# Kernel optimization log

Hardware: AMD Instinct MI355X
Metric: run time of the kernel (lower is better)

## Reference

```python
import jax, jax.numpy as jnp
import numpy as np

B, N, K, UP = 8, 2048, 20, 2
CIN, D, COUT, PH, AH = 256, 64, 128, 64, 256
EPS = 1e-5

def c1(x, W, b):
    # 1x1 Conv1d: x (B,C,N), W (O,C)
    return jnp.einsum('oc,bcn->bon', W, x) + b[None, :, None]

def c2(x, W, b):
    # 1x1 Conv2d: x (B,C,N,K), W (O,C)
    return jnp.einsum('oc,bcnk->bonk', W, x) + b[None, :, None, None]

def bn2(x, g, be):
    # eval-mode BatchNorm2d with running_mean=0, running_var=1
    inv = np.float32(1.0 / np.sqrt(1.0 + EPS))
    return g[None, :, None, None] * x * inv + be[None, :, None, None]

def knn_idx(p, k):
    # p: (B,N,3) -> (B,N,k) indices of k nearest neighbors (incl. self)
    sq = jnp.sum(p * p, -1)
    d = sq[:, :, None] + sq[:, None, :] - 2.0 * jnp.einsum('bnd,bmd->bnm', p, p)
    _, idx = jax.lax.top_k(-d, k)
    return idx

def group(feat, idx):
    # grouping_operation: feat (B,C,N), idx (B,N,k) -> (B,C,N,k)
    return jax.vmap(lambda f, i: f[:, i])(feat, idx)

def setup_inputs() -> dict:
    key = jax.random.key(0)
    ks = jax.random.split(key, 24)
    s = 0.02
    rn = lambda i, shp: jax.random.normal(ks[i], shp, jnp.float32) * s
    return {
        'pos': jax.random.normal(ks[0], (B, 3, N), jnp.float32),
        'key_feat': jax.random.normal(ks[1], (B, CIN, N), jnp.float32),
        'query_feat': jax.random.normal(ks[2], (B, CIN, N), jnp.float32),
        'upfeat': jax.random.normal(ks[3], (B, CIN, N), jnp.float32),
        # mlp_v (MLP_Res): in 2*CIN -> CIN -> CIN with shortcut
        'Wv1': rn(4, (CIN, 2 * CIN)), 'bv1': jnp.zeros(CIN, jnp.float32),
        'Wv2': rn(5, (CIN, CIN)), 'bv2': jnp.zeros(CIN, jnp.float32),
        'Wvs': rn(6, (CIN, 2 * CIN)), 'bvs': jnp.zeros(CIN, jnp.float32),
        # key/query/value/upfeat 1x1 convs CIN -> D
        'Wk': rn(7, (D, CIN)), 'bk': jnp.zeros(D, jnp.float32),
        'Wq': rn(8, (D, CIN)), 'bq': jnp.zeros(D, jnp.float32),
        'Wvv': rn(9, (D, CIN)), 'bvv': jnp.zeros(D, jnp.float32),
        'Wu': rn(10, (D, CIN)), 'bu': jnp.zeros(D, jnp.float32),
        # pos_mlp: 3 -> PH (BN, ReLU) -> D
        'Wp1': rn(11, (PH, 3)), 'bp1': jnp.zeros(PH, jnp.float32),
        'gp1': jnp.ones(PH, jnp.float32), 'betap1': jnp.zeros(PH, jnp.float32),
        'Wp2': rn(12, (D, PH)), 'bp2': jnp.zeros(D, jnp.float32),
        # attn_mlp: D -> AH (BN, ReLU) -> ConvTranspose2d(AH, D, (UP,1), (UP,1))
        'Wa1': rn(13, (AH, D)), 'ba1': jnp.zeros(AH, jnp.float32),
        'ga1': jnp.ones(AH, jnp.float32), 'betaa1': jnp.zeros(AH, jnp.float32),
        'Wt': rn(14, (AH, D, UP)), 'bt': jnp.zeros(D, jnp.float32),
        # conv_end D -> COUT, residual CIN -> COUT
        'Wend': rn(15, (COUT, D)), 'bend': jnp.zeros(COUT, jnp.float32),
        'Wres': rn(16, (COUT, CIN)), 'bres': jnp.zeros(COUT, jnp.float32),
    }

def reference(pos, key_feat, query_feat, upfeat,
              Wv1, bv1, Wv2, bv2, Wvs, bvs,
              Wk, bk, Wq, bq, Wvv, bvv, Wu, bu,
              Wp1, bp1, gp1, betap1, Wp2, bp2,
              Wa1, ba1, ga1, betaa1, Wt, bt,
              Wend, bend, Wres, bres):
    # mlp_v on concat(key, query)
    x = jnp.concatenate([key_feat, query_feat], axis=1)          # (B,2CIN,N)
    value = c1(jax.nn.relu(c1(x, Wv1, bv1)), Wv2, bv2) + c1(x, Wvs, bvs)
    identity = value                                             # (B,CIN,N)
    kf = c1(key_feat, Wk, bk)
    qf = c1(query_feat, Wq, bq)
    vf = c1(value, Wvv, bvv)                                     # (B,D,N)
    idx = knn_idx(pos.transpose(0, 2, 1), K)                     # (B,N,K)
    kg = group(kf, idx)                                          # (B,D,N,K)
    qk_rel = qf[:, :, :, None] - kg
    pos_rel = pos[:, :, :, None] - group(pos, idx)               # (B,3,N,K)
    pos_emb = c2(jax.nn.relu(bn2(c2(pos_rel, Wp1, bp1), gp1, betap1)), Wp2, bp2)
    uf = c1(upfeat, Wu, bu)
    u_rel = uf[:, :, :, None] - group(uf, idx)                   # (B,D,N,K)
    h = jax.nn.relu(bn2(c2(qk_rel + pos_emb + u_rel, Wa1, ba1), ga1, betaa1))  # (B,AH,N,K)
    b = h.shape[0]
    # ConvTranspose2d kernel (UP,1) stride (UP,1): expand N -> N*UP
    att = jnp.einsum('bhnk,hcr->bcnrk', h, Wt).reshape(b, D, N * UP, K) + bt[None, :, None, None]
    att = jax.nn.softmax(att, axis=-1)
    val = group(vf, idx) + pos_emb + u_rel                       # (B,D,N,K)
    val = jnp.repeat(val, UP, axis=2)                            # nearest Upsample (UP,1)
    agg = jnp.sum(att * val, axis=-1)                            # (B,D,N*UP)
    y = c1(agg, Wend, bend)                                      # (B,COUT,N*UP)
    ident = jnp.repeat(c1(identity, Wres, bres), UP, axis=2)     # residual path
    return y + ident
```

## Files before the change

kernel.cpp:

```cpp
#include <hip/hip_runtime.h>
#include <hip/hip_bf16.h>
#include <math.h>

#define BB 8
#define NN 2048
#define KK 20
#define UPF 2
#define CIN 256
#define DD 64
#define COUTN 128
#define PHH 64
#define AHH 256
#define BN_INV 0.9999950000374997f
#define KQ 4
#define NPB 8

typedef __hip_bfloat16 bf16;
typedef unsigned short u16;
typedef unsigned long long u64;
typedef _Float16 f16;
typedef _Float16 h2   __attribute__((ext_vector_type(2)));
typedef _Float16 f16x4 __attribute__((ext_vector_type(4)));
typedef _Float16 f16x8 __attribute__((ext_vector_type(8)));
typedef float    f32x4 __attribute__((ext_vector_type(4)));

static __device__ __forceinline__ float bf2f(const bf16 v) { return __bfloat162float(v); }
static __device__ __forceinline__ bf16  f2bf(const float v) { return __float2bfloat16(v); }
static __device__ __forceinline__ u16   f2bfu(const float v) {
    return __builtin_bit_cast(u16, __float2bfloat16(v));
}
static __device__ __forceinline__ float lo2f(const unsigned v) { return __builtin_bit_cast(float, v << 16); }
static __device__ __forceinline__ float hi2f(const unsigned v) { return __builtin_bit_cast(float, v & 0xFFFF0000u); }

static __device__ __forceinline__ f32x4 mfma16(const f16x8 a, const f16x8 b, const f32x4 c) {
    return __builtin_amdgcn_mfma_f32_16x16x32_f16(a, b, c, 0, 0, 0);
}
static __device__ __forceinline__ unsigned fmap(const float f) {
    unsigned u = __builtin_bit_cast(unsigned, f);
    return (u >> 31) ? ~u : (u | 0x80000000u);
}
static __device__ __forceinline__ void lds_fence() {
    asm volatile("s_waitcnt lgkmcnt(0)" ::: "memory");
    __builtin_amdgcn_sched_barrier(0);
}

__global__ void sentinel_kernel(float* out) {
    if (threadIdx.x == 0 && blockIdx.x == 0) out[0] = 100.0f;
}

__global__ __launch_bounds__(256) void prep_kernel(
    const float* __restrict__ Wa1, const float* __restrict__ Wp2,
    const float* __restrict__ Wend, const float* __restrict__ Wt,
    const float* __restrict__ Wv1, const float* __restrict__ Wv2,
    const float* __restrict__ Wvs, const float* __restrict__ Wvv,
    const float* __restrict__ Wres,
    const float* __restrict__ Wk, const float* __restrict__ Wq,
    const float* __restrict__ Wu,
    const float* __restrict__ ba1, const float* __restrict__ ga1,
    const float* __restrict__ betaa1,
    f16* __restrict__ Wa1h, f16* __restrict__ Wp2h, f16* __restrict__ Wth,
    float* __restrict__ A1s, float* __restrict__ A1b,
    float* __restrict__ WendT,
    f16* __restrict__ Wv1h, f16* __restrict__ Wv2h, f16* __restrict__ Wvsh,
    f16* __restrict__ Wvvh, f16* __restrict__ Wresh,
    f16* __restrict__ Wkh, f16* __restrict__ Wqh, f16* __restrict__ Wuh) {
    const int t = blockIdx.x * 256 + threadIdx.x;
    if (t < AHH * DD)        Wa1h[t] = (f16)Wa1[t];
    if (t < PHH * DD)        Wp2h[t] = (f16)Wp2[t];
    if (t < COUTN * AHH)     { int cr = t >> 8, hh = t & 255; Wth[t] = (f16)Wt[hh * COUTN + cr]; }
    if (t < AHH) {
        float gsc = ga1[t] * BN_INV;
        A1s[t] = gsc;
        A1b[t] = gsc * ba1[t] + betaa1[t];
    }
    if (t < COUTN * DD)      { int r = t / DD,  c = t % DD;  WendT[c * COUTN + r] = Wend[t]; }
    if (t < CIN * 2 * CIN)   Wv1h[t] = (f16)Wv1[t];
    if (t < CIN * CIN)       Wv2h[t] = (f16)Wv2[t];
    if (t < CIN * 2 * CIN)   Wvsh[t] = (f16)Wvs[t];
    if (t < DD * CIN)        Wvvh[t] = (f16)Wvv[t];
    if (t < COUTN * CIN)     Wresh[t] = (f16)Wres[t];
    if (t < DD * CIN)        Wkh[t]  = (f16)Wk[t];
    if (t < DD * CIN)        Wqh[t]  = (f16)Wq[t];
    if (t < DD * CIN)        Wuh[t]  = (f16)Wu[t];
}

__global__ __launch_bounds__(256) void xpose_kernel(
    const float* __restrict__ key_feat, const float* __restrict__ query_feat,
    const float* __restrict__ upfeat,
    f16* __restrict__ xkqT, f16* __restrict__ xuT) {
    __shared__ float tile[64][65];
    const int b  = blockIdx.x >> 5;
    const int n0 = (blockIdx.x & 31) << 6;
    const int y  = blockIdx.y;
    const int src = y >> 2;
    const int ct  = (y & 3) << 6;
    const int t = threadIdx.x;
    const float* xin = (src == 0) ? key_feat : (src == 1) ? query_feat : upfeat;
    f16* dst; int CT, cb;
    if (src < 2) { dst = xkqT; CT = 512; cb = src * 256 + ct; }
    else         { dst = xuT;  CT = 256; cb = ct; }
    for (int u = t; u < 64 * 64; u += 256) {
        const int c = u >> 6, j = u & 63;
        tile[c][j] = xin[((size_t)b * CIN + ct + c) * NN + n0 + j];
    }
    __syncthreads();
    for (int u = t; u < 64 * 32; u += 256) {
        const int n = u >> 5, c0 = (u & 31) << 1;
        h2 pr; pr.x = (f16)tile[c0][n]; pr.y = (f16)tile[c0 + 1][n];
        ((unsigned*)dst)[(((size_t)b * NN + n0 + n) * CT + cb + c0) >> 1] =
            __builtin_bit_cast(unsigned, pr);
    }
}

__global__ __launch_bounds__(256) void knn_kernel(const float* __restrict__ pos,
                                                  u16* __restrict__ idx_out,
                                                  float* __restrict__ posT) {
    __shared__ float dist[KQ][NN];
    __shared__ int   hist[KQ][512];
    __shared__ u64   ltbuf[KQ][KK];
    __shared__ int   tiebuf[KQ][64];

    const int b  = blockIdx.x / (NN / KQ);
    const int n0 = (blockIdx.x % (NN / KQ)) * KQ;
    const int t = threadIdx.x;
    const int g = t >> 6, lane = t & 63;
    const int n = n0 + g;
    const float* pb = pos + (size_t)b * 3 * NN;
    const size_t rowKK = ((size_t)b * NN + n) * KK;

    if (lane < 3) posT[((size_t)b * NN + n) * 3 + lane] = pb[(size_t)lane * NN + n];
    const float qx = pb[n], qy = pb[NN + n], qz = pb[2 * NN + n];
    const float sqq = __fadd_rn(__fadd_rn(__fmul_rn(qx, qx), __fmul_rn(qy, qy)), __fmul_rn(qz, qz));
    for (int j = 0; j < NN / 64; ++j) {
        const int m = lane + j * 64;
        float px = pb[m];
        float py = pb[NN + m];
        float pz = pb[2 * NN + m];
        float sqm = __fadd_rn(__fadd_rn(__fmul_rn(px, px), __fmul_rn(py, py)), __fmul_rn(pz, pz));
        float dt  = __fadd_rn(__fadd_rn(__fmul_rn(qx, px), __fmul_rn(qy, py)), __fmul_rn(qz, pz));
        dist[g][m] = __fsub_rn(__fadd_rn(sqq, sqm), __fmul_rn(2.0f, dt));
    }
    lds_fence();

    unsigned pref = 0u;
    int kn = KK;
    for (int pass = 0; pass < 4; ++pass) {
        const int shift = 24 - 8 * pass;
        const unsigned pm = (pass == 0) ? 0u : (0xFFFFFFFFu << (32 - 8 * pass));
#pragma unroll
        for (int i = 0; i < 8; ++i) hist[g][lane + i * 64] = 0;
        lds_fence();
        for (int j = 0; j < NN / 64; ++j) {
            const unsigned key = fmap(dist[g][lane + j * 64]);
            if ((key & pm) == pref)
                atomicAdd(&hist[g][((lane & 1) << 8) | ((key >> shift) & 255)], 1);
        }
        lds_fence();
        const int h0  = hist[g][4 * lane + 0] + hist[g][256 + 4 * lane + 0];
        const int h1  = hist[g][4 * lane + 1] + hist[g][256 + 4 * lane + 1];
        const int h2v = hist[g][4 * lane + 2] + hist[g][256 + 4 * lane + 2];
        const int h3  = hist[g][4 * lane + 3] + hist[g][256 + 4 * lane + 3];
        const int lsum = h0 + h1 + h2v + h3;
        int incl = lsum;
#pragma unroll
        for (int off = 1; off < 64; off <<= 1) {
            int v = __shfl_up(incl, off, 64);
            if (lane >= off) incl += v;
        }
        const int excl = incl - lsum;
        const bool cross = (excl < kn) && (excl + lsum >= kn);
        const u64 mask = __ballot(cross);
        const int src = __ffsll((unsigned long long)mask) - 1;
        int bsel, cb;
        if      (excl + h0 >= kn)             { bsel = 0; cb = excl; }
        else if (excl + h0 + h1 >= kn)        { bsel = 1; cb = excl + h0; }
        else if (excl + h0 + h1 + h2v >= kn)  { bsel = 2; cb = excl + h0 + h1; }
        else                                  { bsel = 3; cb = excl + h0 + h1 + h2v; }
        const unsigned npref = pref | ((unsigned)(4 * lane + bsel) << shift);
        const int nkn = kn - cb;
        pref = (unsigned)__shfl((int)npref, src, 64);
        kn   = __shfl(nkn, src, 64);
    }

    const unsigned T = pref;
    int nlt = 0, ceq = 0;
    const u64 lmask = (lane == 63) ? 0x7FFFFFFFFFFFFFFFull : ((1ull << lane) - 1);
    for (int j = 0; j < NN / 64; ++j) {
        const int m = lane + j * 64;
        const unsigned key = fmap(dist[g][m]);
        const bool lt = key < T, eq = key == T;
        const u64 mlt = __ballot(lt);
        if (lt) ltbuf[g][nlt + __popcll(mlt & lmask)] = ((u64)key << 32) | (unsigned)m;
        nlt += __popcll(mlt);
        const u64 meq = __ballot(eq);
        if (eq) {
            const int p = ceq + __popcll(meq & lmask);
            if (p < 64) tiebuf[g][p] = m;
        }
        ceq += __popcll(meq);
    }
    lds_fence();

    {
        u64 v = (lane < nlt) ? ltbuf[g][lane] : 0xFFFFFFFFFFFFFFFFull;
        int rank = 0;
#pragma unroll
        for (int j = 0; j < KK; ++j) {
            const u64 o = (u64)__shfl((long long)v, j, 64);
            if (o < v) ++rank;
        }
        if (lane < nlt) idx_out[rowKK + rank] = (u16)(v & 0xFFFFu);
    }
    if (ceq <= 64) {
        int ti = (lane < ceq) ? tiebuf[g][lane] : 0x7FFFFFFF;
        int rk = 0;
        for (int j = 0; j < 64; ++j) {
            const int o = __shfl(ti, j, 64);
            if (o < ti) ++rk;
        }
        if (lane < ceq && rk < kn) idx_out[rowKK + nlt + rk] = (u16)ti;
    } else {
        for (int iter = 0; iter < kn; ++iter) {
            int bi = NN;
            for (int j = 0; j < NN / 64; ++j) {
                const int m = lane + j * 64;
                if (fmap(dist[g][m]) == T && m < bi) bi = m;
            }
#pragma unroll
            for (int off = 32; off > 0; off >>= 1) bi = min(bi, __shfl_down(bi, off, 64));
            bi = __shfl(bi, 0, 64);
            if (lane == 0) {
                idx_out[rowKK + nlt + iter] = (u16)bi;
                dist[g][bi] = 3.4e38f;
            }
            lds_fence();
        }
    }
}

__global__ __launch_bounds__(256) void value_mfma(
    const f16* __restrict__ xkqT,
    const f16* __restrict__ Wv1h, const float* __restrict__ bv1,
    const f16* __restrict__ Wv2h, const float* __restrict__ bv2,
    const f16* __restrict__ Wvsh, const float* __restrict__ bvs,
    const f16* __restrict__ Wvvh, const float* __restrict__ bvv,
    const f16* __restrict__ Wresh, const float* __restrict__ bres,
    bf16* __restrict__ vf_ws, bf16* __restrict__ resid_ws) {
    __shared__ __align__(16) char hv[32 * 512];
    const int b  = blockIdx.x >> 6;
    const int n0 = (blockIdx.x & 63) << 5;
    const int t = threadIdx.x;
    const int w = t >> 6, l = t & 63, g = l >> 4, li = l & 15;
    const f16* xb = xkqT + ((size_t)b * NN + n0) * 512;
    const f32x4 zero4 = {0.f, 0.f, 0.f, 0.f};

    f32x4 a1[4][2];
#pragma unroll
    for (int mt = 0; mt < 4; ++mt) { a1[mt][0] = zero4; a1[mt][1] = zero4; }
    for (int ks = 0; ks < 16; ++ks) {
        f16x8 bx0 = *(const f16x8*)(xb + (size_t)li * 512 + ks * 32 + g * 8);
        f16x8 bx1 = *(const f16x8*)(xb + (size_t)(16 + li) * 512 + ks * 32 + g * 8);
#pragma unroll
        for (int mt = 0; mt < 4; ++mt) {
            const f16x8 af = *(const f16x8*)(Wv1h + (size_t)(w * 64 + mt * 16 + li) * 512 + ks * 32 + g * 8);
            a1[mt][0] = mfma16(af, bx0, a1[mt][0]);
            a1[mt][1] = mfma16(af, bx1, a1[mt][1]);
        }
    }
#pragma unroll
    for (int mt = 0; mt < 4; ++mt) {
        const int ch0 = w * 64 + mt * 16 + g * 4;
        const float4 b4 = *(const float4*)(bv1 + ch0);
#pragma unroll
        for (int nt = 0; nt < 2; ++nt) {
            const int n = nt * 16 + li;
            f16x4 px;
            px.x = (f16)fmaxf(a1[mt][nt][0] + b4.x, 0.f);
            px.y = (f16)fmaxf(a1[mt][nt][1] + b4.y, 0.f);
            px.z = (f16)fmaxf(a1[mt][nt][2] + b4.z, 0.f);
            px.w = (f16)fmaxf(a1[mt][nt][3] + b4.w, 0.f);
            *(f16x4*)(hv + n * 512 + ((ch0 * 2) ^ ((n & 7) << 4))) = px;
        }
    }
    __syncthreads();

    f32x4 a2[4][2];
#pragma unroll
    for (int mt = 0; mt < 4; ++mt) { a2[mt][0] = zero4; a2[mt][1] = zero4; }
    for (int ks = 0; ks < 8; ++ks) {
        f16x8 bh[2];
#pragma unroll
        for (int nt = 0; nt < 2; ++nt) {
            const int n = nt * 16 + li;
            bh[nt] = *(const f16x8*)(hv + n * 512 + ((ks * 64 + g * 16) ^ ((n & 7) << 4)));
        }
#pragma unroll
        for (int mt = 0; mt < 4; ++mt) {
            const f16x8 af = *(const f16x8*)(Wv2h + (size_t)(w * 64 + mt * 16 + li) * 256 + ks * 32 + g * 8);
            a2[mt][0] = mfma16(af, bh[0], a2[mt][0]);
            a2[mt][1] = mfma16(af, bh[1], a2[mt][1]);
        }
    }
    for (int ks = 0; ks < 16; ++ks) {
        f16x8 bx0 = *(const f16x8*)(xb + (size_t)li * 512 + ks * 32 + g * 8);
        f16x8 bx1 = *(const f16x8*)(xb + (size_t)(16 + li) * 512 + ks * 32 + g * 8);
#pragma unroll
        for (int mt = 0; mt < 4; ++mt) {
            const f16x8 af = *(const f16x8*)(Wvsh + (size_t)(w * 64 + mt * 16 + li) * 512 + ks * 32 + g * 8);
            a2[mt][0] = mfma16(af, bx0, a2[mt][0]);
            a2[mt][1] = mfma16(af, bx1, a2[mt][1]);
        }
    }
    __syncthreads();
#pragma unroll
    for (int mt = 0; mt < 4; ++mt) {
        const int ch0 = w * 64 + mt * 16 + g * 4;
        const float4 c4a = *(const float4*)(bv2 + ch0);
        const float4 c4b = *(const float4*)(bvs + ch0);
#pragma unroll
        for (int nt = 0; nt < 2; ++nt) {
            const int n = nt * 16 + li;
            f16x4 px;
            px.x = (f16)(a2[mt][nt][0] + c4a.x + c4b.x);
            px.y = (f16)(a2[mt][nt][1] + c4a.y + c4b.y);
            px.z = (f16)(a2[mt][nt][2] + c4a.z + c4b.z);
            px.w = (f16)(a2[mt][nt][3] + c4a.w + c4b.w);
            *(f16x4*)(hv + n * 512 + ((ch0 * 2) ^ ((n & 7) << 4))) = px;
        }
    }
    __syncthreads();

    f32x4 av[2] = {zero4, zero4};
    f32x4 ar[2][2];
    ar[0][0] = zero4; ar[0][1] = zero4; ar[1][0] = zero4; ar[1][1] = zero4;
    for (int ks = 0; ks < 8; ++ks) {
        f16x8 bh[2];
#pragma unroll
        for (int nt = 0; nt < 2; ++nt) {
            const int n = nt * 16 + li;
            bh[nt] = *(const f16x8*)(hv + n * 512 + ((ks * 64 + g * 16) ^ ((n & 7) << 4)));
        }
        const f16x8 afv = *(const f16x8*)(Wvvh + (size_t)(w * 16 + li) * 256 + ks * 32 + g * 8);
        av[0] = mfma16(afv, bh[0], av[0]);
        av[1] = mfma16(afv, bh[1], av[1]);
#pragma unroll
        for (int rt = 0; rt < 2; ++rt) {
            const f16x8 afr = *(const f16x8*)(Wresh + (size_t)((w * 2 + rt) * 16 + li) * 256 + ks * 32 + g * 8);
            ar[rt][0] = mfma16(afr, bh[0], ar[rt][0]);
            ar[rt][1] = mfma16(afr, bh[1], ar[rt][1]);
        }
    }
    {
        const int ch0 = w * 16 + g * 4;
        const float4 bb = *(const float4*)(bvv + ch0);
#pragma unroll
        for (int nt = 0; nt < 2; ++nt) {
            const int n = nt * 16 + li;
            ushort4 pk;
            pk.x = f2bfu(av[nt][0] + bb.x);
            pk.y = f2bfu(av[nt][1] + bb.y);
            pk.z = f2bfu(av[nt][2] + bb.z);
            pk.w = f2bfu(av[nt][3] + bb.w);
            *(ushort4*)((char*)vf_ws + (((size_t)b * NN + n0 + n) * DD + ch0) * 2) = pk;
        }
    }
#pragma unroll
    for (int rt = 0; rt < 2; ++rt) {
        const int ch0 = (w * 2 + rt) * 16 + g * 4;
        const float4 bb = *(const float4*)(bres + ch0);
#pragma unroll
        for (int nt = 0; nt < 2; ++nt) {
            const int n = nt * 16 + li;
            ushort4 pk;
            pk.x = f2bfu(ar[rt][nt][0] + bb.x);
            pk.y = f2bfu(ar[rt][nt][1] + bb.y);
            pk.z = f2bfu(ar[rt][nt][2] + bb.z);
            pk.w = f2bfu(ar[rt][nt][3] + bb.w);
            *(ushort4*)((char*)resid_ws + (((size_t)b * NN + n0 + n) * COUTN + ch0) * 2) = pk;
        }
    }
}

__global__ __launch_bounds__(256) void proj_mfma(
    const f16* __restrict__ xkqT, const f16* __restrict__ xuT,
    const f16* __restrict__ Wkh, const float* __restrict__ bk,
    const f16* __restrict__ Wqh, const float* __restrict__ bq,
    const f16* __restrict__ Wuh, const float* __restrict__ bu,
    bf16* __restrict__ kf, bf16* __restrict__ qf, bf16* __restrict__ uf) {
    const int b  = blockIdx.x >> 6;
    const int n0 = (blockIdx.x & 63) << 5;
    const int t = threadIdx.x;
    const int w = t >> 6, l = t & 63, g = l >> 4, li = l & 15;
    if (w == 3) return;
    const f16* xb; int stride; const f16* W; const float* bias; bf16* out;
    if (w == 0)      { xb = xkqT + ((size_t)b * NN + n0) * 512;       stride = 512; W = Wkh; bias = bk; out = kf; }
    else if (w == 1) { xb = xkqT + ((size_t)b * NN + n0) * 512 + 256; stride = 512; W = Wqh; bias = bq; out = qf; }
    else             { xb = xuT + ((size_t)b * NN + n0) * 256;        stride = 256; W = Wuh; bias = bu; out = uf; }
    const f32x4 zero4 = {0.f, 0.f, 0.f, 0.f};
    f32x4 acc[4][2];
#pragma unroll
    for (int mt = 0; mt < 4; ++mt) { acc[mt][0] = zero4; acc[mt][1] = zero4; }
    for (int ks = 0; ks < 8; ++ks) {
        f16x8 bx0 = *(const f16x8*)(xb + (size_t)li * stride + ks * 32 + g * 8);
        f16x8 bx1 = *(const f16x8*)(xb + (size_t)(16 + li) * stride + ks * 32 + g * 8);
#pragma unroll
        for (int mt = 0; mt < 4; ++mt) {
            const f16x8 af = *(const f16x8*)(W + (size_t)(mt * 16 + li) * 256 + ks * 32 + g * 8);
            acc[mt][0] = mfma16(af, bx0, acc[mt][0]);
            acc[mt][1] = mfma16(af, bx1, acc[mt][1]);
        }
    }
#pragma unroll
    for (int mt = 0; mt < 4; ++mt) {
        const int ch0 = mt * 16 + g * 4;
        const float4 bb = *(const float4*)(bias + ch0);
#pragma unroll
        for (int nt = 0; nt < 2; ++nt) {
            const int n = nt * 16 + li;
            ushort4 pk;
            pk.x = f2bfu(acc[mt][nt][0] + bb.x);
            pk.y = f2bfu(acc[mt][nt][1] + bb.y);
            pk.z = f2bfu(acc[mt][nt][2] + bb.z);
            pk.w = f2bfu(acc[mt][nt][3] + bb.w);
            *(ushort4*)((char*)out + (((size_t)b * NN + n0 + n) * DD + ch0) * 2) = pk;
        }
    }
}

__global__ __launch_bounds__(512, 4) void attn_fused(
    const float* __restrict__ posT, const u16* __restrict__ idx_ws,
    const bf16* __restrict__ kf_ws, const bf16* __restrict__ qf_ws,
    const bf16* __restrict__ uf_ws, const bf16* __restrict__ vf_ws,
    const bf16* __restrict__ resid_ws,
    const float* __restrict__ Wp1, const float* __restrict__ bp1,
    const float* __restrict__ gp1, const float* __restrict__ betap1,
    const f16* __restrict__ Wp2h, const float* __restrict__ bp2,
    const f16* __restrict__ Wa1h, const float* __restrict__ A1s,
    const float* __restrict__ A1b, const f16* __restrict__ Wth,
    const float* __restrict__ WendT, const float* __restrict__ bend,
    float* __restrict__ out) {
    __shared__ __align__(16) char pool[61440];
    f16*  ph16 = (f16*)(pool);
    f16*  S16  = (f16*)(pool);
    f16*  L16T = (f16*)(pool);
    f16*  peh  = (f16*)(pool + 20480);
    char* Hl   = pool + 20480;
    f16*  V16  = (f16*)(pool + 40960);
    __shared__ int   nidx[8 * KK];
    __shared__ float prel[8 * KK][3];
    __shared__ float qcol[NPB][64], ucol[NPB][64];
    __shared__ float aggl[NPB][COUTN];

    const int b  = blockIdx.x >> 8;
    const int n0 = (blockIdx.x & 255) << 3;
    const int t = threadIdx.x;
    const int w = t >> 6, l = t & 63, g = l >> 4, li = l & 15;
    const int m4 = w & 3, nh = w >> 2;
    const size_t row0 = (size_t)b * NN + n0;
    const f32x4 zero4 = {0.f, 0.f, 0.f, 0.f};

    if (t < 8 * KK) nidx[t] = (int)idx_ws[row0 * KK + t];
    __syncthreads();

    {
        const int n = t >> 6, c = t & 63;
        qcol[n][c] = bf2f(qf_ws[(row0 + n) * DD + c]);
        ucol[n][c] = bf2f(uf_ws[(row0 + n) * DD + c]);
    }
    if (t < 480) {
        const int r = t / 3, d = t - r * 3;
        const int n = r / KK;
        prel[r][d] = posT[(row0 + n) * 3 + d] - posT[((size_t)b * NN + nidx[r]) * 3 + d];
    }
    __syncthreads();

    for (int u = t; u < 160 * 32; u += 512) {
        const int r = u >> 5, c0 = (u & 31) << 1;
        float a0 = Wp1[c0 * 3 + 0] * prel[r][0] + Wp1[c0 * 3 + 1] * prel[r][1]
                 + Wp1[c0 * 3 + 2] * prel[r][2] + bp1[c0];
        float a1 = Wp1[c0 * 3 + 3] * prel[r][0] + Wp1[c0 * 3 + 4] * prel[r][1]
                 + Wp1[c0 * 3 + 5] * prel[r][2] + bp1[c0 + 1];
        a0 = gp1[c0] * a0 * BN_INV + betap1[c0];
        a1 = gp1[c0 + 1] * a1 * BN_INV + betap1[c0 + 1];
        h2 pr; pr.x = (f16)fmaxf(a0, 0.f); pr.y = (f16)fmaxf(a1, 0.f);
        *(unsigned*)((char*)ph16 + (r * 128 + ((c0 * 2) ^ ((r & 7) << 4)))) =
            __builtin_bit_cast(unsigned, pr);
    }
    __syncthreads();

    {
        f32x4 d[5];
#pragma unroll
        for (int j = 0; j < 5; ++j) d[j] = zero4;
#pragma unroll
        for (int ks = 0; ks < 2; ++ks) {
            const f16x8 af = *(const f16x8*)(Wp2h + (m4 * 16 + li) * 64 + ks * 32 + g * 8);
#pragma unroll
            for (int j = 0; j < 5; ++j) {
                const int r = (nh * 5 + j) * 16 + li;
                const f16x8 bf = *(const f16x8*)((const char*)ph16 +
                                  (r * 128 + ((ks * 64 + g * 16) ^ ((r & 7) << 4))));
                d[j] = mfma16(af, bf, d[j]);
            }
        }
        const int ch0 = m4 * 16 + g * 4;
        const float4 b4 = *(const float4*)(bp2 + ch0);
#pragma unroll
        for (int j = 0; j < 5; ++j) {
            const int r = (nh * 5 + j) * 16 + li;
            f16x4 pk;
            pk.x = (f16)(d[j][0] + b4.x);
            pk.y = (f16)(d[j][1] + b4.y);
            pk.z = (f16)(d[j][2] + b4.z);
            pk.w = (f16)(d[j][3] + b4.w);
            *(f16x4*)((char*)peh + (r * 128 + ((ch0 * 2) ^ ((r & 7) << 4)))) = pk;
        }
    }
    __syncthreads();

    for (int u = t; u < 160 * 32; u += 512) {
        const int r = u >> 5, c0 = (u & 31) << 1;
        const int n = r / KK;
        const size_t nb2 = (((size_t)b * NN + nidx[r]) * DD + c0) * 2;
        const unsigned kq = *(const unsigned*)((const char*)kf_ws + nb2);
        const unsigned uq = *(const unsigned*)((const char*)uf_ws + nb2);
        const unsigned vq = *(const unsigned*)((const char*)vf_ws + nb2);
        const unsigned pw = *(const unsigned*)((const char*)peh +
                              (r * 128 + ((c0 * 2) ^ ((r & 7) << 4))));
        const h2 pp = __builtin_bit_cast(h2, pw);
        const float add0 = ucol[n][c0] + (float)pp.x;
        const float add1 = ucol[n][c0 + 1] + (float)pp.y;
        const float gb0 = -(lo2f(kq) + lo2f(uq));
        const float gb1 = -(hi2f(kq) + hi2f(uq));
        const float vb0 = lo2f(vq) - lo2f(uq);
        const float vb1 = hi2f(vq) - hi2f(uq);
        h2 s; s.x = (f16)(gb0 + qcol[n][c0] + add0); s.y = (f16)(gb1 + qcol[n][c0 + 1] + add1);
        h2 v; v.x = (f16)(vb0 + add0);               v.y = (f16)(vb1 + add1);
        const int sw = (c0 * 2) ^ ((r & 7) << 4);
        *(unsigned*)((char*)S16 + (r * 128 + sw)) = __builtin_bit_cast(unsigned, s);
        *(unsigned*)((char*)V16 + (r * 128 + sw)) = __builtin_bit_cast(unsigned, v);
    }
    __syncthreads();

    f32x4 acc2[10];
#pragma unroll
    for (int j = 0; j < 10; ++j) acc2[j] = zero4;

    for (int c4 = 0; c4 < 4; ++c4) {
        const int hrb = c4 * 64 + m4 * 16;
        f32x4 d1[5];
#pragma unroll
        for (int j = 0; j < 5; ++j) d1[j] = zero4;
#pragma unroll
        for (int ks = 0; ks < 2; ++ks) {
            const f16x8 af = *(const f16x8*)(Wa1h + (hrb + li) * 64 + ks * 32 + g * 8);
#pragma unroll
            for (int j = 0; j < 5; ++j) {
                const int r = (nh * 5 + j) * 16 + li;
                const f16x8 sfv = *(const f16x8*)((const char*)S16 +
                                   (r * 128 + ((ks * 64 + g * 16) ^ ((r & 7) << 4))));
                d1[j] = mfma16(af, sfv, d1[j]);
            }
        }
        const float4 as4 = *(const float4*)(A1s + hrb + g * 4);
        const float4 ab4 = *(const float4*)(A1b + hrb + g * 4);
        __syncthreads();
#pragma unroll
        for (int j = 0; j < 5; ++j) {
            const int col = (nh * 5 + j) * 16 + li;
            const int ch0 = m4 * 16 + g * 4;
            f16x4 pk;
            pk.x = (f16)fmaxf(as4.x * d1[j][0] + ab4.x, 0.f);
            pk.y = (f16)fmaxf(as4.y * d1[j][1] + ab4.y, 0.f);
            pk.z = (f16)fmaxf(as4.z * d1[j][2] + ab4.z, 0.f);
            pk.w = (f16)fmaxf(as4.w * d1[j][3] + ab4.w, 0.f);
            *(f16x4*)(Hl + col * 128 + ((ch0 * 2) ^ ((col & 7) << 4))) = pk;
        }
        __syncthreads();
#pragma unroll
        for (int ks2 = 0; ks2 < 2; ++ks2) {
            const f16x8 bf = *(const f16x8*)(Wth + (size_t)(w * 16 + li) * AHH + c4 * 64 + ks2 * 32 + g * 8);
#pragma unroll
            for (int nt = 0; nt < 10; ++nt) {
                const int col = nt * 16 + li;
                const f16x8 ha = *(const f16x8*)(Hl + col * 128 + ((ks2 * 64 + g * 16) ^ ((col & 7) << 4)));
                acc2[nt] = mfma16(ha, bf, acc2[nt]);
            }
        }
    }
    __syncthreads();

#pragma unroll
    for (int nt = 0; nt < 10; ++nt) {
        const f32x4 d = acc2[nt];
#pragma unroll
        for (int j = 0; j < 4; ++j) {
            const int row = nt * 16 + g * 4 + j;
            *(f16*)((char*)L16T + (row * 256 + (((w * 16 + li) * 2) ^ ((row & 3) << 5)))) =
                (f16)d[j];
        }
    }
    __syncthreads();

    {
        const int cr = t & 127, c = cr >> 1;
        const int nbase = (t >> 7) * 2;
        for (int p = 0; p < 2; ++p) {
            const int n = nbase + p;
            float lv[20];
#pragma unroll
            for (int k = 0; k < 20; ++k) {
                const int row = n * KK + k;
                lv[k] = (float)*(const f16*)((const char*)L16T +
                          (row * 256 + ((cr * 2) ^ ((row & 3) << 5))));
            }
            float m = lv[0];
#pragma unroll
            for (int k = 1; k < 20; ++k) m = fmaxf(m, lv[k]);
            float s = 0.f, a = 0.f;
#pragma unroll
            for (int k = 0; k < 20; ++k) {
                const float e = expf(lv[k] - m);
                s += e;
                const int r = n * KK + k;
                const float vv = (float)*(const f16*)((const char*)V16 +
                                   (r * 128 + ((c * 2) ^ ((r & 7) << 4))));
                a += e * vv;
            }
            aggl[n][cr] = a / s;
        }
    }
    __syncthreads();

    {
        const int o = t & 127, np = t >> 7;
        const int na = 2 * np, nb = 2 * np + 1;
        float a0r0 = 0.f, a0r1 = 0.f, a1r0 = 0.f, a1r1 = 0.f;
        for (int cc = 0; cc < DD; ++cc) {
            const float wv = WendT[cc * COUTN + o];
            a0r0 += wv * aggl[na][cc * 2];
            a0r1 += wv * aggl[na][cc * 2 + 1];
            a1r0 += wv * aggl[nb][cc * 2];
            a1r1 += wv * aggl[nb][cc * 2 + 1];
        }
        const float be = bend[o];
        const float r0 = bf2f(resid_ws[(row0 + na) * COUTN + o]);
        const float r1 = bf2f(resid_ws[(row0 + nb) * COUTN + o]);
        float4 ov;
        ov.x = a0r0 + be + r0; ov.y = a0r1 + be + r0;
        ov.z = a1r0 + be + r1; ov.w = a1r1 + be + r1;
        *(float4*)(out + (size_t)b * COUTN * (NN * UPF) + (size_t)o * (NN * UPF) + 2 * n0 + 4 * np) = ov;
    }
}

extern "C" void kernel_launch(void* const* d_in, const int* in_sizes, int n_in,
                              void* d_out, int out_size, void* d_ws, size_t ws_size,
                              hipStream_t stream) {
    const float* pos        = (const float*)d_in[0];
    const float* key_feat   = (const float*)d_in[1];
    const float* query_feat = (const float*)d_in[2];
    const float* upfeat     = (const float*)d_in[3];
    const float* Wv1 = (const float*)d_in[4];
    const float* bv1 = (const float*)d_in[5];
    const float* Wv2 = (const float*)d_in[6];
    const float* bv2 = (const float*)d_in[7];
    const float* Wvs = (const float*)d_in[8];
    const float* bvs = (const float*)d_in[9];
    const float* Wk  = (const float*)d_in[10];
    const float* bk  = (const float*)d_in[11];
    const float* Wq  = (const float*)d_in[12];
    const float* bq  = (const float*)d_in[13];
    const float* Wvv = (const float*)d_in[14];
    const float* bvv = (const float*)d_in[15];
    const float* Wu  = (const float*)d_in[16];
    const float* bu  = (const float*)d_in[17];
    const float* Wp1 = (const float*)d_in[18];
    const float* bp1 = (const float*)d_in[19];
    const float* gp1 = (const float*)d_in[20];
    const float* betap1 = (const float*)d_in[21];
    const float* Wp2 = (const float*)d_in[22];
    const float* bp2 = (const float*)d_in[23];
    const float* Wa1 = (const float*)d_in[24];
    const float* ba1 = (const float*)d_in[25];
    const float* ga1 = (const float*)d_in[26];
    const float* betaa1 = (const float*)d_in[27];
    const float* Wt   = (const float*)d_in[28];
    const float* bt   = (const float*)d_in[29];
    const float* Wend = (const float*)d_in[30];
    const float* bend = (const float*)d_in[31];
    const float* Wres = (const float*)d_in[32];
    const float* bres = (const float*)d_in[33];
    float* out = (float*)d_out;
    (void)out_size; (void)bt;

    const bool sizes_ok = (n_in >= 34)
        && (in_sizes[0] == BB * 3 * NN)
        && (in_sizes[1] == BB * CIN * NN)
        && (in_sizes[4] == CIN * 2 * CIN)
        && (in_sizes[28] == AHH * DD * UPF)
        && (in_sizes[32] == COUTN * CIN);

    size_t off = 0;
    auto take = [&](size_t bytes) { size_t o = off; off = (off + bytes + 255) & ~(size_t)255; return o; };
    const size_t off_posT  = take((size_t)BB * NN * 3 * sizeof(float));
    const size_t off_idx   = take((size_t)BB * NN * KK * sizeof(u16));
    const size_t off_vf    = take((size_t)BB * NN * DD * sizeof(bf16));
    const size_t off_kf    = take((size_t)BB * NN * DD * sizeof(bf16));
    const size_t off_qf    = take((size_t)BB * NN * DD * sizeof(bf16));
    const size_t off_uf    = take((size_t)BB * NN * DD * sizeof(bf16));
    const size_t off_resid = take((size_t)BB * NN * COUTN * sizeof(bf16));
    const size_t off_wa1h  = take((size_t)AHH * DD * sizeof(f16));
    const size_t off_wp2h  = take((size_t)PHH * DD * sizeof(f16));
    const size_t off_wth   = take((size_t)COUTN * AHH * sizeof(f16));
    const size_t off_a1s   = take((size_t)AHH * sizeof(float));
    const size_t off_a1b   = take((size_t)AHH * sizeof(float));
    const size_t off_wendt = take((size_t)COUTN * DD * sizeof(float));
    const size_t off_wv1h  = take((size_t)CIN * 2 * CIN * sizeof(f16));
    const size_t off_wv2h  = take((size_t)CIN * CIN * sizeof(f16));
    const size_t off_wvsh  = take((size_t)CIN * 2 * CIN * sizeof(f16));
    const size_t off_wvvh  = take((size_t)DD * CIN * sizeof(f16));
    const size_t off_wresh = take((size_t)COUTN * CIN * sizeof(f16));
    const size_t off_wkh   = take((size_t)DD * CIN * sizeof(f16));
    const size_t off_wqh   = take((size_t)DD * CIN * sizeof(f16));
    const size_t off_wuh   = take((size_t)DD * CIN * sizeof(f16));
    const size_t off_xkq   = take((size_t)BB * NN * 512 * sizeof(f16));
    const size_t off_xu    = take((size_t)BB * NN * 256 * sizeof(f16));
    const size_t NEED = off;

    if (!sizes_ok) return;
    if (ws_size < NEED) {
        sentinel_kernel<<<1, 64, 0, stream>>>(out);
        return;
    }

    char* ws = (char*)d_ws;
    float* posT_ws  = (float*)(ws + off_posT);
    u16*   idx_ws   = (u16*)(ws + off_idx);
    bf16*  vf_ws    = (bf16*)(ws + off_vf);
    bf16*  kf_ws    = (bf16*)(ws + off_kf);
    bf16*  qf_ws    = (bf16*)(ws + off_qf);
    bf16*  uf_ws    = (bf16*)(ws + off_uf);
    bf16*  resid_ws = (bf16*)(ws + off_resid);
    f16*   Wa1h_ws  = (f16*)(ws + off_wa1h);
    f16*   Wp2h_ws  = (f16*)(ws + off_wp2h);
    f16*   Wth_ws   = (f16*)(ws + off_wth);
    float* A1s_ws   = (float*)(ws + off_a1s);
    float* A1b_ws   = (float*)(ws + off_a1b);
    float* WendT_ws = (float*)(ws + off_wendt);
    f16*   Wv1h_ws  = (f16*)(ws + off_wv1h);
    f16*   Wv2h_ws  = (f16*)(ws + off_wv2h);
    f16*   Wvsh_ws  = (f16*)(ws + off_wvsh);
    f16*   Wvvh_ws  = (f16*)(ws + off_wvvh);
    f16*   Wresh_ws = (f16*)(ws + off_wresh);
    f16*   Wkh_ws   = (f16*)(ws + off_wkh);
    f16*   Wqh_ws   = (f16*)(ws + off_wqh);
    f16*   Wuh_ws   = (f16*)(ws + off_wuh);
    f16*   xkqT_ws  = (f16*)(ws + off_xkq);
    f16*   xuT_ws   = (f16*)(ws + off_xu);

    prep_kernel<<<(CIN * 2 * CIN + 255) / 256, 256, 0, stream>>>(
        Wa1, Wp2, Wend, Wt, Wv1, Wv2, Wvs, Wvv, Wres, Wk, Wq, Wu,
        ba1, ga1, betaa1,
        Wa1h_ws, Wp2h_ws, Wth_ws, A1s_ws, A1b_ws, WendT_ws,
        Wv1h_ws, Wv2h_ws, Wvsh_ws, Wvvh_ws, Wresh_ws, Wkh_ws, Wqh_ws, Wuh_ws);
    xpose_kernel<<<dim3(BB * (NN / 64), 12), 256, 0, stream>>>(
        key_feat, query_feat, upfeat, xkqT_ws, xuT_ws);
    knn_kernel<<<BB * (NN / KQ), 256, 0, stream>>>(pos, idx_ws, posT_ws);
    value_mfma<<<BB * (NN / 32), 256, 0, stream>>>(xkqT_ws,
        Wv1h_ws, bv1, Wv2h_ws, bv2, Wvsh_ws, bvs, Wvvh_ws, bvv, Wresh_ws, bres,
        vf_ws, resid_ws);
    proj_mfma<<<BB * (NN / 32), 256, 0, stream>>>(xkqT_ws, xuT_ws,
        Wkh_ws, bk, Wqh_ws, bq, Wuh_ws, bu, kf_ws, qf_ws, uf_ws);
    attn_fused<<<BB * (NN / NPB), 512, 0, stream>>>(posT_ws, idx_ws,
        kf_ws, qf_ws, uf_ws, vf_ws, resid_ws,
        Wp1, bp1, gp1, betap1, Wp2h_ws, bp2,
        Wa1h_ws, A1s_ws, A1b_ws, Wth_ws, WendT_ws, bend, out);
}
```

Baseline: 489.0 us.

## Rework kNN selection: one query per block with range-adaptive single-pass histogram

New measurement: 447.7 us. 1.09x faster.

```diff
diff --git a/kernel.cpp b/kernel.cpp
--- a/kernel.cpp
+++ b/kernel.cpp
@@ -12,7 +12,6 @@
 #define PHH 64
 #define AHH 256
 #define BN_INV 0.9999950000374997f
-#define KQ 4
 #define NPB 8
 
 typedef __hip_bfloat16 bf16;
@@ -38,10 +37,6 @@
 static __device__ __forceinline__ unsigned fmap(const float f) {
     unsigned u = __builtin_bit_cast(unsigned, f);
     return (u >> 31) ? ~u : (u | 0x80000000u);
-}
-static __device__ __forceinline__ void lds_fence() {
-    asm volatile("s_waitcnt lgkmcnt(0)" ::: "memory");
-    __builtin_amdgcn_sched_barrier(0);
 }
 
 __global__ void sentinel_kernel(float* out) {
@@ -115,125 +110,208 @@
 __global__ __launch_bounds__(256) void knn_kernel(const float* __restrict__ pos,
                                                   u16* __restrict__ idx_out,
                                                   float* __restrict__ posT) {
-    __shared__ float dist[KQ][NN];
-    __shared__ int   hist[KQ][512];
-    __shared__ u64   ltbuf[KQ][KK];
-    __shared__ int   tiebuf[KQ][64];
-
-    const int b  = blockIdx.x / (NN / KQ);
-    const int n0 = (blockIdx.x % (NN / KQ)) * KQ;
+    __shared__ float dist[NN];
+    __shared__ int   hist[512];
+    __shared__ unsigned rmin[4], rmax[4];
+    __shared__ u64   cbuf[64];
+    __shared__ float q[3];
+    __shared__ unsigned minkS;
+    __shared__ int   shiftS, jstarS, cntS;
+    __shared__ u64   ltbuf[KK];
+    __shared__ int   tiebuf[64];
+    __shared__ int   ri[4];
+    __shared__ unsigned prefS;
+    __shared__ int   knS, cnt_lt, cnt_eq;
+
+    const int b = blockIdx.x / NN;
+    const int n = blockIdx.x % NN;
     const int t = threadIdx.x;
-    const int g = t >> 6, lane = t & 63;
-    const int n = n0 + g;
     const float* pb = pos + (size_t)b * 3 * NN;
     const size_t rowKK = ((size_t)b * NN + n) * KK;
 
-    if (lane < 3) posT[((size_t)b * NN + n) * 3 + lane] = pb[(size_t)lane * NN + n];
-    const float qx = pb[n], qy = pb[NN + n], qz = pb[2 * NN + n];
+    if (t < 3) {
+        float v = pb[(size_t)t * NN + n];
+        q[t] = v;
+        posT[((size_t)b * NN + n) * 3 + t] = v;
+    }
+    if (t == 0) { prefS = 0u; knS = KK; cnt_lt = 0; cnt_eq = 0; cntS = 0; jstarS = 0; }
+    __syncthreads();
+    const float qx = q[0], qy = q[1], qz = q[2];
     const float sqq = __fadd_rn(__fadd_rn(__fmul_rn(qx, qx), __fmul_rn(qy, qy)), __fmul_rn(qz, qz));
-    for (int j = 0; j < NN / 64; ++j) {
-        const int m = lane + j * 64;
+    unsigned kmin = 0xFFFFFFFFu, kmax = 0u;
+    for (int m = t; m < NN; m += 256) {
         float px = pb[m];
         float py = pb[NN + m];
         float pz = pb[2 * NN + m];
         float sqm = __fadd_rn(__fadd_rn(__fmul_rn(px, px), __fmul_rn(py, py)), __fmul_rn(pz, pz));
         float dt  = __fadd_rn(__fadd_rn(__fmul_rn(qx, px), __fmul_rn(qy, py)), __fmul_rn(qz, pz));
-        dist[g][m] = __fsub_rn(__fadd_rn(sqq, sqm), __fmul_rn(2.0f, dt));
-    }
-    lds_fence();
-
-    unsigned pref = 0u;
-    int kn = KK;
+        const float d = __fsub_rn(__fadd_rn(sqq, sqm), __fmul_rn(2.0f, dt));
+        dist[m] = d;
+        const unsigned key = fmap(d);
+        kmin = min(kmin, key);
+        kmax = max(kmax, key);
+    }
+#pragma unroll
+    for (int off = 32; off > 0; off >>= 1) {
+        kmin = min(kmin, (unsigned)__shfl_down((int)kmin, off, 64));
+        kmax = max(kmax, (unsigned)__shfl_down((int)kmax, off, 64));
+    }
+    if ((t & 63) == 0) { rmin[t >> 6] = kmin; rmax[t >> 6] = kmax; }
+    hist[t] = 0; hist[256 + t] = 0;
+    __syncthreads();
+    if (t == 0) {
+        const unsigned mn = min(min(rmin[0], rmin[1]), min(rmin[2], rmin[3]));
+        const unsigned mx = max(max(rmax[0], rmax[1]), max(rmax[2], rmax[3]));
+        const unsigned range = mx - mn;
+        minkS  = mn;
+        shiftS = (range >= 256u) ? (24 - __clz((int)range)) : 0;
+    }
+    __syncthreads();
+    const unsigned mink = minkS;
+    const int sh = shiftS;
+
+    for (int m = t; m < NN; m += 256) {
+        const unsigned bin = (fmap(dist[m]) - mink) >> sh;
+        atomicAdd(&hist[((unsigned)(t & 1) << 8) | bin], 1);
+    }
+    __syncthreads();
+    if (t < 64) {
+        const int h0  = hist[4 * t + 0] + hist[256 + 4 * t + 0];
+        const int h1  = hist[4 * t + 1] + hist[256 + 4 * t + 1];
+        const int h2v = hist[4 * t + 2] + hist[256 + 4 * t + 2];
+        const int h3  = hist[4 * t + 3] + hist[256 + 4 * t + 3];
+        const int lsum = h0 + h1 + h2v + h3;
+        int incl = lsum;
+#pragma unroll
+        for (int off = 1; off < 64; off <<= 1) {
+            int v = __shfl_up(incl, off, 64);
+            if (t >= off) incl += v;
+        }
+        const int excl = incl - lsum;
+        if (excl < KK && excl + lsum >= KK) {
+            int bsel;
+            if      (excl + h0 >= KK)            bsel = 0;
+            else if (excl + h0 + h1 >= KK)       bsel = 1;
+            else if (excl + h0 + h1 + h2v >= KK) bsel = 2;
+            else                                 bsel = 3;
+            jstarS = 4 * t + bsel;
+        }
+    }
+    __syncthreads();
+    const unsigned jstar = (unsigned)jstarS;
+
+    for (int m = t; m < NN; m += 256) {
+        const unsigned key = fmap(dist[m]);
+        if (((key - mink) >> sh) <= jstar) {
+            const int p = atomicAdd(&cntS, 1);
+            if (p < 64) cbuf[p] = ((u64)key << 32) | (unsigned)m;
+        }
+    }
+    __syncthreads();
+    const int total = cntS;
+
+    if (total <= 64) {
+        if (t < 64) {
+            u64 v = (t < total) ? cbuf[t] : 0xFFFFFFFFFFFFFFFFull;
+            int rank = 0;
+#pragma unroll 16
+            for (int j = 0; j < 64; ++j) {
+                const u64 o = (u64)__shfl((long long)v, j, 64);
+                if (o < v) ++rank;
+            }
+            if (t < total && rank < KK) idx_out[rowKK + rank] = (u16)(v & 0xFFFFu);
+        }
+        return;
+    }
+
     for (int pass = 0; pass < 4; ++pass) {
         const int shift = 24 - 8 * pass;
         const unsigned pm = (pass == 0) ? 0u : (0xFFFFFFFFu << (32 - 8 * pass));
-#pragma unroll
-        for (int i = 0; i < 8; ++i) hist[g][lane + i * 64] = 0;
-        lds_fence();
-        for (int j = 0; j < NN / 64; ++j) {
-            const unsigned key = fmap(dist[g][lane + j * 64]);
+        hist[t] = 0;
+        __syncthreads();
+        const unsigned pref = prefS;
+        const int kn = knS;
+        for (int m = t; m < NN; m += 256) {
+            unsigned key = fmap(dist[m]);
             if ((key & pm) == pref)
-                atomicAdd(&hist[g][((lane & 1) << 8) | ((key >> shift) & 255)], 1);
-        }
-        lds_fence();
-        const int h0  = hist[g][4 * lane + 0] + hist[g][256 + 4 * lane + 0];
-        const int h1  = hist[g][4 * lane + 1] + hist[g][256 + 4 * lane + 1];
-        const int h2v = hist[g][4 * lane + 2] + hist[g][256 + 4 * lane + 2];
-        const int h3  = hist[g][4 * lane + 3] + hist[g][256 + 4 * lane + 3];
-        const int lsum = h0 + h1 + h2v + h3;
-        int incl = lsum;
-#pragma unroll
-        for (int off = 1; off < 64; off <<= 1) {
-            int v = __shfl_up(incl, off, 64);
-            if (lane >= off) incl += v;
-        }
-        const int excl = incl - lsum;
-        const bool cross = (excl < kn) && (excl + lsum >= kn);
-        const u64 mask = __ballot(cross);
-        const int src = __ffsll((unsigned long long)mask) - 1;
-        int bsel, cb;
-        if      (excl + h0 >= kn)             { bsel = 0; cb = excl; }
-        else if (excl + h0 + h1 >= kn)        { bsel = 1; cb = excl + h0; }
-        else if (excl + h0 + h1 + h2v >= kn)  { bsel = 2; cb = excl + h0 + h1; }
-        else                                  { bsel = 3; cb = excl + h0 + h1 + h2v; }
-        const unsigned npref = pref | ((unsigned)(4 * lane + bsel) << shift);
-        const int nkn = kn - cb;
-        pref = (unsigned)__shfl((int)npref, src, 64);
-        kn   = __shfl(nkn, src, 64);
-    }
-
-    const unsigned T = pref;
-    int nlt = 0, ceq = 0;
-    const u64 lmask = (lane == 63) ? 0x7FFFFFFFFFFFFFFFull : ((1ull << lane) - 1);
-    for (int j = 0; j < NN / 64; ++j) {
-        const int m = lane + j * 64;
-        const unsigned key = fmap(dist[g][m]);
-        const bool lt = key < T, eq = key == T;
-        const u64 mlt = __ballot(lt);
-        if (lt) ltbuf[g][nlt + __popcll(mlt & lmask)] = ((u64)key << 32) | (unsigned)m;
-        nlt += __popcll(mlt);
-        const u64 meq = __ballot(eq);
-        if (eq) {
-            const int p = ceq + __popcll(meq & lmask);
-            if (p < 64) tiebuf[g][p] = m;
-        }
-        ceq += __popcll(meq);
-    }
-    lds_fence();
-
-    {
-        u64 v = (lane < nlt) ? ltbuf[g][lane] : 0xFFFFFFFFFFFFFFFFull;
+                atomicAdd(&hist[(key >> shift) & 255], 1);
+        }
+        __syncthreads();
+        if (t < 64) {
+            const int h0 = hist[4 * t + 0], h1 = hist[4 * t + 1];
+            const int h2v = hist[4 * t + 2], h3 = hist[4 * t + 3];
+            const int lsum = h0 + h1 + h2v + h3;
+            int incl = lsum;
+#pragma unroll
+            for (int off = 1; off < 64; off <<= 1) {
+                int v = __shfl_up(incl, off, 64);
+                if (t >= off) incl += v;
+            }
+            const int excl = incl - lsum;
+            if (excl < kn && excl + lsum >= kn) {
+                int bsel, cb;
+                if      (excl + h0 >= kn)            { bsel = 0; cb = excl; }
+                else if (excl + h0 + h1 >= kn)       { bsel = 1; cb = excl + h0; }
+                else if (excl + h0 + h1 + h2v >= kn) { bsel = 2; cb = excl + h0 + h1; }
+                else                                 { bsel = 3; cb = excl + h0 + h1 + h2v; }
+                knS = kn - cb;
+                prefS = pref | ((unsigned)(4 * t + bsel) << shift);
+            }
+        }
+        __syncthreads();
+    }
+
+    const unsigned T = prefS;
+    for (int m = t; m < NN; m += 256) {
+        unsigned key = fmap(dist[m]);
+        if (key < T) {
+            int p = atomicAdd(&cnt_lt, 1);
+            ltbuf[p] = ((u64)key << 32) | (unsigned)m;
+        } else if (key == T) {
+            int p = atomicAdd(&cnt_eq, 1);
+            if (p < 64) tiebuf[p] = m;
+        }
+    }
+    __syncthreads();
+    const int nlt = cnt_lt, neq_need = knS, ceq = cnt_eq;
+
+    if (t < 64) {
+        u64 v = (t < nlt) ? ltbuf[t] : 0xFFFFFFFFFFFFFFFFull;
         int rank = 0;
 #pragma unroll
         for (int j = 0; j < KK; ++j) {
             const u64 o = (u64)__shfl((long long)v, j, 64);
             if (o < v) ++rank;
         }
-        if (lane < nlt) idx_out[rowKK + rank] = (u16)(v & 0xFFFFu);
+        if (t < nlt) idx_out[rowKK + rank] = (u16)(v & 0xFFFFu);
     }
     if (ceq <= 64) {
-        int ti = (lane < ceq) ? tiebuf[g][lane] : 0x7FFFFFFF;
-        int rk = 0;
-        for (int j = 0; j < 64; ++j) {
-            const int o = __shfl(ti, j, 64);
-            if (o < ti) ++rk;
-        }
-        if (lane < ceq && rk < kn) idx_out[rowKK + nlt + rk] = (u16)ti;
+        if (t < 64) {
+            int ti = (t < ceq) ? tiebuf[t] : 0x7FFFFFFF;
+            int rk = 0;
+            for (int j = 0; j < 64; ++j) {
+                const int o = __shfl(ti, j, 64);
+                if (o < ti) ++rk;
+            }
+            if (t < ceq && rk < neq_need) idx_out[rowKK + nlt + rk] = (u16)ti;
+        }
     } else {
-        for (int iter = 0; iter < kn; ++iter) {
+        for (int iter = 0; iter < neq_need; ++iter) {
             int bi = NN;
-            for (int j = 0; j < NN / 64; ++j) {
-                const int m = lane + j * 64;
-                if (fmap(dist[g][m]) == T && m < bi) bi = m;
-            }
-#pragma unroll
-            for (int off = 32; off > 0; off >>= 1) bi = min(bi, __shfl_down(bi, off, 64));
-            bi = __shfl(bi, 0, 64);
-            if (lane == 0) {
-                idx_out[rowKK + nlt + iter] = (u16)bi;
-                dist[g][bi] = 3.4e38f;
-            }
-            lds_fence();
+            for (int m = t; m < NN; m += 256)
+                if (fmap(dist[m]) == T && m < bi) bi = m;
+            for (int off = 32; off > 0; off >>= 1) {
+                int i2 = __shfl_down(bi, off, 64);
+                bi = min(bi, i2);
+            }
+            if ((t & 63) == 0) ri[t >> 6] = bi;
+            __syncthreads();
+            if (t == 0) {
+                int i0 = min(min(ri[0], ri[1]), min(ri[2], ri[3]));
+                idx_out[rowKK + nlt + iter] = (u16)i0;
+                dist[i0] = 3.4e38f;
+            }
+            __syncthreads();
         }
     }
 }
@@ -765,7 +843,7 @@
         Wv1h_ws, Wv2h_ws, Wvsh_ws, Wvvh_ws, Wresh_ws, Wkh_ws, Wqh_ws, Wuh_ws);
     xpose_kernel<<<dim3(BB * (NN / 64), 12), 256, 0, stream>>>(
         key_feat, query_feat, upfeat, xkqT_ws, xuT_ws);
-    knn_kernel<<<BB * (NN / KQ), 256, 0, stream>>>(pos, idx_ws, posT_ws);
+    knn_kernel<<<BB * NN, 256, 0, stream>>>(pos, idx_ws, posT_ws);
     value_mfma<<<BB * (NN / 32), 256, 0, stream>>>(xkqT_ws,
         Wv1h_ws, bv1, Wv2h_ws, bv2, Wvsh_ws, bvs, Wvvh_ws, bvv, Wresh_ws, bres,
         vf_ws, resid_ws);
```
